# Kernel optimization log

Measured on AMD Instinct MI355X. Metric: run time of the kernel, lower is better.

The kernel has to match this reference:

```python
import jax, jax.numpy as jnp
import numpy as np
import math

B, LQ, LK, D, H = 4, 1024, 1024, 1024, 16
DK = D // H
SCALE = 1.0 / math.sqrt(DK)
NEG_INF = -1.0e9


def setup_inputs() -> dict:
    key = jax.random.key(0)
    ks = jax.random.split(key, 18)
    w = lambda k: (jax.random.normal(k, (D, D), dtype=jnp.float32) * 0.02)
    b = lambda k: (jax.random.normal(k, (D,), dtype=jnp.float32) * 0.02)
    mask = jax.random.randint(ks[4], (B, 1, LK), 0, 2).astype(jnp.int32)
    mask = mask.at[..., 0].set(1)  # ensure at least one valid key per row
    return {
        "query": jax.random.normal(ks[0], (B, LQ, D), dtype=jnp.float32),
        "key": jax.random.normal(ks[1], (B, LK, D), dtype=jnp.float32),
        "value": jax.random.normal(ks[2], (B, LK, D), dtype=jnp.float32),
        "weak_rela": jax.random.normal(ks[3], (B, LK, D), dtype=jnp.float32),
        "mask": mask,
        "Wq": w(ks[5]), "bq": b(ks[6]),
        "Wk": w(ks[7]), "bk": b(ks[8]),
        "Wv": w(ks[9]), "bv": b(ks[10]),
        "Wrk": w(ks[11]), "brk": b(ks[12]),
        "Wrv": w(ks[13]), "brv": b(ks[14]),
        "Wo": w(ks[15]), "bo": b(ks[16]),
    }


def _proj(x, W, bias):
    # x: [B, L, D] -> [B, H, L, DK]; torch Linear: y = x @ W.T + b
    y = x @ W.T + bias
    Bn, L, _ = y.shape
    return y.reshape(Bn, L, H, DK).transpose(0, 2, 1, 3)


def reference(query, key, value, weak_rela, mask,
              Wq, bq, Wk, bk, Wv, bv, Wrk, brk, Wrv, brv, Wo, bo):
    q = _proj(query, Wq, bq)        # [B,H,LQ,DK]
    k = _proj(key, Wk, bk)          # [B,H,LK,DK]
    v = _proj(value, Wv, bv)        # [B,H,LK,DK]
    rk = _proj(weak_rela, Wrk, brk) # [B,H,LK,DK]
    rv = _proj(weak_rela, Wrv, brv) # [B,H,LK,DK]

    qk = jnp.einsum('bhqd,bhkd->bhqk', q, k) * SCALE
    qr = jnp.einsum('bhqd,bhkd->bhqk', q, rk) * SCALE

    m = (mask[:, None, :, :] == 0)  # [B,1,1,LK] broadcast over heads/queries
    qk = jnp.where(m, NEG_INF, qk)
    qr = jnp.where(m, NEG_INF, qr)

    p_vis = jax.nn.softmax(qk, axis=-1)
    p_rel = jax.nn.softmax(qr, axis=-1)

    x = (jnp.einsum('bhqk,bhkd->bhqd', p_vis, v)
         + jnp.einsum('bhqk,bhkd->bhqd', p_rel, rv))  # [B,H,LQ,DK]
    x = x.transpose(0, 2, 1, 3).reshape(query.shape[0], -1, H * DK)
    return x @ Wo.T + bo
```

## Files before the change

### kernel.cpp

```cpp
#include <hip/hip_runtime.h>
#include <stdint.h>

#define NB 4
#define NH 16
#define DKH 64
#define DMODEL 1024
#define SEQ 1024
#define SCALE 0.125f
#define NEG_INF -1.0e9f
#define K2E 0.18033688011112042f

typedef __bf16 bf16_t;
typedef __bf16 bf16x8 __attribute__((ext_vector_type(8)));
typedef __bf16 bf16x4v __attribute__((ext_vector_type(4)));
typedef float f32x4 __attribute__((ext_vector_type(4)));
typedef uint32_t u32x4 __attribute__((ext_vector_type(4)));

typedef const uint32_t __attribute__((address_space(1)))* gas_ptr;
typedef uint32_t __attribute__((address_space(3)))* las_ptr;

__device__ __forceinline__ void gload_lds16(const void* g, void* l) {
  __builtin_amdgcn_global_load_lds((gas_ptr)g, (las_ptr)l, 16, 0, 0);
}


#define NXE ((size_t)NB * SEQ * DMODEL)
#define NWE ((size_t)DMODEL * DMODEL)

__global__ void cvt_all(const float* __restrict__ x0, const float* __restrict__ x1,
                        const float* __restrict__ x2, const float* __restrict__ x3,
                        const float* __restrict__ w0, const float* __restrict__ w1,
                        const float* __restrict__ w2, const float* __restrict__ w3,
                        const float* __restrict__ w4, const float* __restrict__ w5,
                        bf16_t* __restrict__ Xbase, bf16_t* __restrict__ Wbase) {
  const int y = blockIdx.y;
  const float* in;
  bf16_t* out;
  int n;
  if (y < 4) {
    in = (y == 0) ? x0 : (y == 1) ? x1 : (y == 2) ? x2 : x3;
    out = Xbase + (size_t)y * NXE;
    n = (int)NXE;
  } else {
    const int j = y - 4;
    in = (j == 0) ? w0 : (j == 1) ? w1 : (j == 2) ? w2 : (j == 3) ? w3 : (j == 4) ? w4 : w5;
    out = Wbase + (size_t)j * NWE;
    n = (int)NWE;
  }
  const int idx = (blockIdx.x * 256 + threadIdx.x) * 4;
  if (idx >= n) return;
  const float4 v = *(const float4*)(in + idx);
  bf16x4v p;
  p[0] = (bf16_t)v.x; p[1] = (bf16_t)v.y; p[2] = (bf16_t)v.z; p[3] = (bf16_t)v.w;
  *(bf16x4v*)(out + idx) = p;
}

template<int MODE>
__device__ __forceinline__ void gemm128_body(
    const bf16_t* __restrict__ A, const bf16_t* __restrict__ W,
    const float* __restrict__ bias, void* __restrict__ outp,
    int m0, int n0, bf16_t* As, bf16_t* Bs) {
  const int tid = threadIdx.x;
  const int lane = tid & 63;
  const int w = tid >> 6;
  const int wm = w >> 1, wn = w & 1;
  const int g = lane >> 4, c = lane & 15;
  const int lrow = lane >> 3;
  const int lcol = ((lane & 7) * 8) ^ ((lane >> 3) << 3);
  const int sc = (c & 7) << 3;

  f32x4 acc[4][4] = {};

  for (int kt = 0; kt < DMODEL; kt += 64) {
#pragma unroll
    for (int p = 0; p < 4; ++p) {
      const int row = w * 32 + p * 8;
      gload_lds16(A + (size_t)(m0 + row + lrow) * DMODEL + kt + lcol, &As[row * 64]);
      gload_lds16(W + (size_t)(n0 + row + lrow) * DMODEL + kt + lcol, &Bs[row * 64]);
    }
    __syncthreads();
    bf16x8 af[4][2], bfr[4][2];
#pragma unroll
    for (int i = 0; i < 4; ++i)
#pragma unroll
      for (int kk = 0; kk < 2; ++kk) {
        af[i][kk]  = *(const bf16x8*)&As[(wm * 64 + i * 16 + c) * 64 + ((kk * 32 + g * 8) ^ sc)];
        bfr[i][kk] = *(const bf16x8*)&Bs[(wn * 64 + i * 16 + c) * 64 + ((kk * 32 + g * 8) ^ sc)];
      }
#pragma unroll
    for (int i = 0; i < 4; ++i)
#pragma unroll
      for (int j = 0; j < 4; ++j) {
        acc[i][j] = __builtin_amdgcn_mfma_f32_16x16x32_bf16(af[i][0], bfr[j][0], acc[i][j], 0, 0, 0);
        acc[i][j] = __builtin_amdgcn_mfma_f32_16x16x32_bf16(af[i][1], bfr[j][1], acc[i][j], 0, 0, 0);
      }
    __syncthreads();
  }

  float bv4[4];
#pragma unroll
  for (int j = 0; j < 4; ++j) bv4[j] = bias[n0 + wn * 64 + j * 16 + c];

#pragma unroll
  for (int i = 0; i < 4; ++i) {
    const int mrow = m0 + wm * 64 + i * 16 + g * 4;
    const int b_ = mrow >> 10, l_ = mrow & 1023;
#pragma unroll
    for (int j = 0; j < 4; ++j) {
      const int n = n0 + wn * 64 + j * 16 + c;
      if (MODE == 0) {
        bf16_t* o = (bf16_t*)outp;
        const int h_ = n >> 6, dk_ = n & 63;
#pragma unroll
        for (int r = 0; r < 4; ++r)
          o[((size_t)(b_ * NH + h_) * SEQ + l_ + r) * DKH + dk_] =
              (bf16_t)(acc[i][j][r] + bv4[j]);
      } else {
        bf16_t* o = (bf16_t*)outp;
        const int h_ = n >> 6, dk_ = n & 63;
        bf16x4v pk;
#pragma unroll
        for (int r = 0; r < 4; ++r) pk[r] = (bf16_t)(acc[i][j][r] + bv4[j]);
        *(bf16x4v*)&o[((size_t)(b_ * NH + h_) * DKH + dk_) * SEQ + l_] = pk;
      }
    }
  }
}

__global__ void __launch_bounds__(256, 2)
proj_gemm(const bf16_t* __restrict__ Xbase, const bf16_t* __restrict__ Wbase,
          bf16_t* __restrict__ Obase,
          const float* __restrict__ b0, const float* __restrict__ b1,
          const float* __restrict__ b2, const float* __restrict__ b3,
          const float* __restrict__ b4) {
  __shared__ bf16_t As[128 * 64];
  __shared__ bf16_t Bs[128 * 64];
  const int bid = blockIdx.x;
  const int lid = (bid & 7) * 160 + (bid >> 3);
  const int seg = lid >> 8;
  const int rr = lid & 255;
  const int m0 = (rr >> 3) * 128, n0 = (rr & 7) * 128;

  const bf16_t* A = Xbase + (size_t)((seg < 3) ? seg : 3) * NXE;
  const bf16_t* W = Wbase + (size_t)seg * NWE;
  const int ooff = (seg == 0) ? 0 : (seg == 1) ? 1 : (seg == 2) ? 3 : (seg == 3) ? 2 : 4;
  bf16_t* out = Obase + (size_t)ooff * NXE;
  const float* bias = (seg == 0) ? b0 : (seg == 1) ? b1 : (seg == 2) ? b2 : (seg == 3) ? b3 : b4;

  if (seg == 2 || seg == 4) gemm128_body<1>(A, W, bias, out, m0, n0, As, Bs);
  else                      gemm128_body<0>(A, W, bias, out, m0, n0, As, Bs);
}

__global__ void __launch_bounds__(256, 2)
out_gemm(const bf16_t* __restrict__ A, const bf16_t* __restrict__ W,
         const float* __restrict__ bias, float* __restrict__ out) {
  __shared__ bf16_t As[128 * 64];
  __shared__ bf16_t Bs[64 * 64];
  const int tid = threadIdx.x;
  const int lane = tid & 63;
  const int w = tid >> 6;
  const int wm = w >> 1, wn = w & 1;
  const int g = lane >> 4, c = lane & 15;
  const int bid = blockIdx.x;
  const int lid = (bid & 7) * 64 + (bid >> 3);
  const int bm = lid >> 4, bn = lid & 15;
  const int m0 = bm * 128, n0 = bn * 64;
  const int lrow = lane >> 3;
  const int lcol = ((lane & 7) * 8) ^ ((lane >> 3) << 3);
  const int sc = (c & 7) << 3;

  f32x4 acc[4][2] = {};

  for (int kt = 0; kt < DMODEL; kt += 64) {
#pragma unroll
    for (int p = 0; p < 4; ++p) {
      const int row = w * 32 + p * 8;
      gload_lds16(A + (size_t)(m0 + row + lrow) * DMODEL + kt + lcol, &As[row * 64]);
    }
#pragma unroll
    for (int p = 0; p < 2; ++p) {
      const int row = w * 16 + p * 8;
      gload_lds16(W + (size_t)(n0 + row + lrow) * DMODEL + kt + lcol, &Bs[row * 64]);
    }
    __syncthreads();
    bf16x8 af[4][2], bfr[2][2];
#pragma unroll
    for (int i = 0; i < 4; ++i)
#pragma unroll
      for (int kk = 0; kk < 2; ++kk)
        af[i][kk] = *(const bf16x8*)&As[(wm * 64 + i * 16 + c) * 64 + ((kk * 32 + g * 8) ^ sc)];
#pragma unroll
    for (int j = 0; j < 2; ++j)
#pragma unroll
      for (int kk = 0; kk < 2; ++kk)
        bfr[j][kk] = *(const bf16x8*)&Bs[(wn * 32 + j * 16 + c) * 64 + ((kk * 32 + g * 8) ^ sc)];
#pragma unroll
    for (int i = 0; i < 4; ++i)
#pragma unroll
      for (int j = 0; j < 2; ++j) {
        acc[i][j] = __builtin_amdgcn_mfma_f32_16x16x32_bf16(af[i][0], bfr[j][0], acc[i][j], 0, 0, 0);
        acc[i][j] = __builtin_amdgcn_mfma_f32_16x16x32_bf16(af[i][1], bfr[j][1], acc[i][j], 0, 0, 0);
      }
    __syncthreads();
  }

  float bv2[2];
#pragma unroll
  for (int j = 0; j < 2; ++j) bv2[j] = bias[n0 + wn * 32 + j * 16 + c];
#pragma unroll
  for (int i = 0; i < 4; ++i) {
    const int mrow = m0 + wm * 64 + i * 16 + g * 4;
#pragma unroll
    for (int j = 0; j < 2; ++j) {
      const int n = n0 + wn * 32 + j * 16 + c;
#pragma unroll
      for (int r = 0; r < 4; ++r)
        out[(size_t)(mrow + r) * DMODEL + n] = acc[i][j][r] + bv2[j];
    }
  }
}

__global__ void __launch_bounds__(256, 2)
attn_kernel(const bf16_t* __restrict__ q, const bf16_t* __restrict__ k,
            const bf16_t* __restrict__ rk, const bf16_t* __restrict__ vT,
            const bf16_t* __restrict__ rvT, const int* __restrict__ mask,
            bf16_t* __restrict__ x) {
  extern __shared__ __align__(256) bf16_t smem[];
  bf16_t* Ks  = smem;
  bf16_t* RKs = Ks  + 64 * 64;
  bf16_t* Vs  = RKs + 64 * 64;
  bf16_t* RVs = Vs  + 64 * 64;
  bf16_t* Pbase = RVs + 64 * 64;
  float* Mb = (float*)(Pbase + 8 * 2048);

  const int tid = threadIdx.x;
  const int lane = tid & 63;
  const int w = tid >> 6;
  const int g = lane >> 4, c = lane & 15;
  const int sc = (c & 7) << 3;
  const int bid = blockIdx.x;
  const int lid = (bid & 7) * 64 + (bid >> 3);
  const int qt = lid & 7;
  const int bh = lid >> 3;
  const int b = bh >> 4, h = bh & 15;
  const int q0 = qt * 128;

  const bf16_t* qp = q + (size_t)bh * SEQ * DKH;
  const bf16_t* kp = k + (size_t)bh * SEQ * DKH;
  const bf16_t* rkp = rk + (size_t)bh * SEQ * DKH;
  const bf16_t* vp = vT + (size_t)bh * DKH * SEQ;
  const bf16_t* rvp = rvT + (size_t)bh * DKH * SEQ;
  const int* mp = mask + b * SEQ;

  const int lrow = lane >> 3;
  const int lcolL = (lane & 7) * 8;
  const int wcol = lcolL ^ (((w * 16 + lrow) & 7) << 3);

  bf16_t* Pwv = Pbase + w * 2048;
  bf16_t* Pwr = Pbase + (4 + w) * 2048;

#pragma unroll
  for (int i = 0; i < 4; ++i) {
    const int idx = i * 256 + tid;
    Mb[idx] = (mp[idx] == 0) ? NEG_INF : 0.0f;
  }

  bf16x8 qf[2][2];
#pragma unroll
  for (int i = 0; i < 2; ++i)
#pragma unroll
    for (int kk = 0; kk < 2; ++kk)
      qf[i][kk] = *(const bf16x8*)(qp + (size_t)(q0 + w * 32 + i * 16 + c) * DKH + kk * 32 + g * 8);

  f32x4 ov[2][4] = {}, orl[2][4] = {};
  float mv[2] = {NEG_INF, NEG_INF}, mr[2] = {NEG_INF, NEG_INF};
  float lv[2] = {0.f, 0.f}, lr[2] = {0.f, 0.f};

  u32x4 st[4][2];

  auto ldreg = [&](int kv0) {
#pragma unroll
    for (int p = 0; p < 2; ++p) {
      const int row = w * 16 + p * 8 + lrow;
      st[0][p] = *(const u32x4*)(kp  + (size_t)(kv0 + row) * DKH + lcolL);
      st[1][p] = *(const u32x4*)(rkp + (size_t)(kv0 + row) * DKH + lcolL);
      st[2][p] = *(const u32x4*)(vp  + (size_t)row * SEQ + kv0 + lcolL);
      st[3][p] = *(const u32x4*)(rvp + (size_t)row * SEQ + kv0 + lcolL);
    }
  };
  auto wrlds = [&]() {
#pragma unroll
    for (int p = 0; p < 2; ++p) {
      const int row = w * 16 + p * 8 + lrow;
      *(u32x4*)&Ks [row * 64 + wcol] = st[0][p];
      *(u32x4*)&RKs[row * 64 + wcol] = st[1][p];
      *(u32x4*)&Vs [row * 64 + wcol] = st[2][p];
      *(u32x4*)&RVs[row * 64 + wcol] = st[3][p];
    }
  };

  auto qk_sm = [&](const bf16_t* Kt, bf16_t* Pb, const f32x4 (&mb)[4],
                   float (&m_s)[2], float (&l_s)[2], f32x4 (&o_s)[2][4]) {
    f32x4 s[2][4];
    {
      bf16x8 kfr[4][2];
#pragma unroll
      for (int f = 0; f < 4; ++f) {
        kfr[f][0] = *(const bf16x8*)&Kt[(f * 16 + c) * 64 + ((g * 8) ^ sc)];
        kfr[f][1] = *(const bf16x8*)&Kt[(f * 16 + c) * 64 + ((32 + g * 8) ^ sc)];
      }
      __builtin_amdgcn_s_setprio(1);
#pragma unroll
      for (int i = 0; i < 2; ++i)
#pragma unroll
        for (int f = 0; f < 4; ++f) {
          f32x4 a = {0.f, 0.f, 0.f, 0.f};
          a = __builtin_amdgcn_mfma_f32_16x16x32_bf16(kfr[f][0], qf[i][0], a, 0, 0, 0);
          a = __builtin_amdgcn_mfma_f32_16x16x32_bf16(kfr[f][1], qf[i][1], a, 0, 0, 0);
          s[i][f] = a;
        }
      __builtin_amdgcn_s_setprio(0);
    }

#pragma unroll
    for (int i = 0; i < 2; ++i)
#pragma unroll
      for (int f = 0; f < 4; ++f)
#pragma unroll
        for (int r = 0; r < 4; ++r)
          s[i][f][r] = s[i][f][r] * K2E + mb[f][r];

#pragma unroll
    for (int i = 0; i < 2; ++i) {
      float tm = fmaxf(fmaxf(s[i][0][0], s[i][0][1]), fmaxf(s[i][0][2], s[i][0][3]));
#pragma unroll
      for (int f = 1; f < 4; ++f)
        tm = fmaxf(tm, fmaxf(fmaxf(s[i][f][0], s[i][f][1]), fmaxf(s[i][f][2], s[i][f][3])));
      tm = fmaxf(tm, __shfl_xor(tm, 16));
      tm = fmaxf(tm, __shfl_xor(tm, 32));
      if (!__all(tm <= m_s[i] + 8.0f)) {
        const float mnew = fmaxf(m_s[i], tm);
        const float sf = __builtin_amdgcn_exp2f(m_s[i] - mnew);
        m_s[i] = mnew;
        l_s[i] *= sf;
#pragma unroll
        for (int jd = 0; jd < 4; ++jd)
#pragma unroll
          for (int r = 0; r < 4; ++r) o_s[i][jd][r] *= sf;
      }
      float pf = 0.f;
#pragma unroll
      for (int f = 0; f < 4; ++f) {
        bf16x4v pk;
#pragma unroll
        for (int r = 0; r < 4; ++r) {
          const float p = __builtin_amdgcn_exp2f(s[i][f][r] - m_s[i]);
          pf += p;
          pk[r] = (bf16_t)p;
        }
        *(bf16x4v*)&Pb[i * 1024 + c * 64 + ((f * 16 + g * 4) ^ sc)] = pk;
      }
      l_s[i] += pf;
    }
  };

  auto pv = [&](const bf16_t* Vt, const bf16_t* Pb, f32x4 (&o_s)[2][4]) {
    bf16x8 pa[2][2];
#pragma unroll
    for (int i = 0; i < 2; ++i) {
      pa[i][0] = *(const bf16x8*)&Pb[i * 1024 + c * 64 + ((g * 8) ^ sc)];
      pa[i][1] = *(const bf16x8*)&Pb[i * 1024 + c * 64 + ((32 + g * 8) ^ sc)];
    }
#pragma unroll
    for (int jd = 0; jd < 4; ++jd) {
      const bf16x8 v0 = *(const bf16x8*)&Vt[(jd * 16 + c) * 64 + ((g * 8) ^ sc)];
      const bf16x8 v1 = *(const bf16x8*)&Vt[(jd * 16 + c) * 64 + ((32 + g * 8) ^ sc)];
#pragma unroll
      for (int i = 0; i < 2; ++i) {
        o_s[i][jd] = __builtin_amdgcn_mfma_f32_16x16x32_bf16(v0, pa[i][0], o_s[i][jd], 0, 0, 0);
        o_s[i][jd] = __builtin_amdgcn_mfma_f32_16x16x32_bf16(v1, pa[i][1], o_s[i][jd], 0, 0, 0);
      }
    }
  };

  ldreg(0);
  wrlds();
  __syncthreads();

  for (int t = 0; t < 16; ++t) {
    const int kv0 = t * 64;

    if (t < 15) ldreg(kv0 + 64);

    f32x4 mb[4];
#pragma unroll
    for (int f = 0; f < 4; ++f)
      mb[f] = *(const f32x4*)&Mb[kv0 + f * 16 + g * 4];

    qk_sm(Ks,  Pwv, mb, mv, lv, ov);
    qk_sm(RKs, Pwr, mb, mr, lr, orl);
    __builtin_amdgcn_s_setprio(1);
    pv(Vs,  Pwv, ov);
    pv(RVs, Pwr, orl);
    __builtin_amdgcn_s_setprio(0);

    if (t < 15) {
      __syncthreads();
      wrlds();
      __syncthreads();
    }
  }

#pragma unroll
  for (int i = 0; i < 2; ++i) {
    lv[i] += __shfl_xor(lv[i], 16); lv[i] += __shfl_xor(lv[i], 32);
    lr[i] += __shfl_xor(lr[i], 16); lr[i] += __shfl_xor(lr[i], 32);
  }

  bf16_t* xb = x + (size_t)b * SEQ * DMODEL + (size_t)h * DKH;
#pragma unroll
  for (int i = 0; i < 2; ++i) {
    const float rlv = 1.0f / lv[i], rlr = 1.0f / lr[i];
    const int qrow = q0 + w * 32 + i * 16 + c;
#pragma unroll
    for (int jd = 0; jd < 4; ++jd) {
      bf16x4v pk;
#pragma unroll
      for (int r = 0; r < 4; ++r)
        pk[r] = (bf16_t)(ov[i][jd][r] * rlv + orl[i][jd][r] * rlr);
      *(bf16x4v*)&xb[(size_t)qrow * DMODEL + jd * 16 + g * 4] = pk;
    }
  }
}

extern "C" void kernel_launch(void* const* d_in, const int* in_sizes, int n_in,
                              void* d_out, int out_size, void* d_ws, size_t ws_size,
                              hipStream_t stream) {
  (void)in_sizes; (void)n_in; (void)out_size; (void)ws_size;
  const float* query = (const float*)d_in[0];
  const float* key_  = (const float*)d_in[1];
  const float* value = (const float*)d_in[2];
  const float* weak  = (const float*)d_in[3];
  const int*   mask  = (const int*)d_in[4];
  const float* Wq  = (const float*)d_in[5];  const float* bq  = (const float*)d_in[6];
  const float* Wk  = (const float*)d_in[7];  const float* bk  = (const float*)d_in[8];
  const float* Wv  = (const float*)d_in[9];  const float* bv  = (const float*)d_in[10];
  const float* Wrk = (const float*)d_in[11]; const float* brk = (const float*)d_in[12];
  const float* Wrv = (const float*)d_in[13]; const float* brv = (const float*)d_in[14];
  const float* Wo  = (const float*)d_in[15]; const float* bo  = (const float*)d_in[16];

  char* ws = (char*)d_ws;
  size_t off = 0;
  auto alloc = [&](size_t bytes) {
    void* p = ws + off;
    off += (bytes + 255) & ~(size_t)255;
    return p;
  };
  const size_t SZ_X = NXE * sizeof(bf16_t);
  const size_t SZ_W = NWE * sizeof(bf16_t);

  bf16_t* Xq = (bf16_t*)alloc(SZ_X);
  bf16_t* Xk = (bf16_t*)alloc(SZ_X);
  bf16_t* Xv = (bf16_t*)alloc(SZ_X);
  bf16_t* Xr = (bf16_t*)alloc(SZ_X);
  bf16_t* Wqb  = (bf16_t*)alloc(SZ_W);
  bf16_t* Wkb  = (bf16_t*)alloc(SZ_W);
  bf16_t* Wvb  = (bf16_t*)alloc(SZ_W);
  bf16_t* Wrkb = (bf16_t*)alloc(SZ_W);
  bf16_t* Wrvb = (bf16_t*)alloc(SZ_W);
  bf16_t* Wob  = (bf16_t*)alloc(SZ_W);
  bf16_t* qh   = (bf16_t*)alloc(SZ_X);
  bf16_t* kh   = (bf16_t*)alloc(SZ_X);
  bf16_t* rkh  = (bf16_t*)alloc(SZ_X);
  bf16_t* vTh  = (bf16_t*)alloc(SZ_X);
  bf16_t* rvTh = (bf16_t*)alloc(SZ_X);
  bf16_t* xh   = (bf16_t*)alloc(SZ_X);
  (void)Xk; (void)Xv; (void)Xr; (void)Wkb; (void)Wvb; (void)Wrkb; (void)Wrvb;
  (void)kh; (void)rkh; (void)vTh; (void)rvTh;

  cvt_all<<<dim3(4096, 10), 256, 0, stream>>>(query, key_, value, weak,
                                              Wq, Wk, Wv, Wrk, Wrv, Wo,
                                              Xq, Wqb);

  proj_gemm<<<dim3(1280), 256, 0, stream>>>(Xq, Wqb, qh, bq, bk, bv, brk, brv);

  attn_kernel<<<dim3(512), 256, 69632, stream>>>(qh, kh, rkh, vTh, rvTh, mask, xh);

  out_gemm<<<dim3(512), 256, 0, stream>>>(xh, Wob, bo, (float*)d_out);
}
```

Baseline: 161.7 us.

## Double-buffer K/V tiles in LDS with two-deep register prefetch

The attention loop now ping-pongs between two LDS buffers holding K, RK, V and RV. It prefetches global tiles two steps ahead into registers, which cuts the two barriers per iteration down to one. The mask is read from global into registers and turned into bias values each step, replacing the LDS mask table. The visible and relation branches now run qk then pv in sequence and share one per-wave P buffer. LDS use rises to 80 KB per block, which leaves only just enough room for two blocks per CU, and register pressure goes up from the extra prefetch state.

```diff
diff --git a/kernel.cpp b/kernel.cpp
--- a/kernel.cpp
+++ b/kernel.cpp
@@ -226,12 +226,7 @@
             const bf16_t* __restrict__ rvT, const int* __restrict__ mask,
             bf16_t* __restrict__ x) {
   extern __shared__ __align__(256) bf16_t smem[];
-  bf16_t* Ks  = smem;
-  bf16_t* RKs = Ks  + 64 * 64;
-  bf16_t* Vs  = RKs + 64 * 64;
-  bf16_t* RVs = Vs  + 64 * 64;
-  bf16_t* Pbase = RVs + 64 * 64;
-  float* Mb = (float*)(Pbase + 8 * 2048);
+  bf16_t* Pbase = smem + 2 * 16384;
 
   const int tid = threadIdx.x;
   const int lane = tid & 63;
@@ -256,14 +251,7 @@
   const int lcolL = (lane & 7) * 8;
   const int wcol = lcolL ^ (((w * 16 + lrow) & 7) << 3);
 
-  bf16_t* Pwv = Pbase + w * 2048;
-  bf16_t* Pwr = Pbase + (4 + w) * 2048;
-
-#pragma unroll
-  for (int i = 0; i < 4; ++i) {
-    const int idx = i * 256 + tid;
-    Mb[idx] = (mp[idx] == 0) ? NEG_INF : 0.0f;
-  }
+  bf16_t* Pw = Pbase + w * 2048;
 
   bf16x8 qf[2][2];
 #pragma unroll
@@ -277,6 +265,8 @@
   float lv[2] = {0.f, 0.f}, lr[2] = {0.f, 0.f};
 
   u32x4 st[4][2];
+  int4 st_m[4];
+  int4 mk[4];
 
   auto ldreg = [&](int kv0) {
 #pragma unroll
@@ -287,19 +277,22 @@
       st[2][p] = *(const u32x4*)(vp  + (size_t)row * SEQ + kv0 + lcolL);
       st[3][p] = *(const u32x4*)(rvp + (size_t)row * SEQ + kv0 + lcolL);
     }
-  };
-  auto wrlds = [&]() {
+#pragma unroll
+    for (int f = 0; f < 4; ++f)
+      st_m[f] = *(const int4*)&mp[kv0 + f * 16 + g * 4];
+  };
+  auto wrlds = [&](bf16_t* buf) {
 #pragma unroll
     for (int p = 0; p < 2; ++p) {
       const int row = w * 16 + p * 8 + lrow;
-      *(u32x4*)&Ks [row * 64 + wcol] = st[0][p];
-      *(u32x4*)&RKs[row * 64 + wcol] = st[1][p];
-      *(u32x4*)&Vs [row * 64 + wcol] = st[2][p];
-      *(u32x4*)&RVs[row * 64 + wcol] = st[3][p];
-    }
-  };
-
-  auto qk_sm = [&](const bf16_t* Kt, bf16_t* Pb, const f32x4 (&mb)[4],
+      *(u32x4*)&buf[0 * 4096 + row * 64 + wcol] = st[0][p];
+      *(u32x4*)&buf[1 * 4096 + row * 64 + wcol] = st[1][p];
+      *(u32x4*)&buf[2 * 4096 + row * 64 + wcol] = st[2][p];
+      *(u32x4*)&buf[3 * 4096 + row * 64 + wcol] = st[3][p];
+    }
+  };
+
+  auto qk_sm = [&](const bf16_t* Kt, const f32x4 (&mb)[4],
                    float (&m_s)[2], float (&l_s)[2], f32x4 (&o_s)[2][4]) {
     f32x4 s[2][4];
     {
@@ -309,7 +302,6 @@
         kfr[f][0] = *(const bf16x8*)&Kt[(f * 16 + c) * 64 + ((g * 8) ^ sc)];
         kfr[f][1] = *(const bf16x8*)&Kt[(f * 16 + c) * 64 + ((32 + g * 8) ^ sc)];
       }
-      __builtin_amdgcn_s_setprio(1);
 #pragma unroll
       for (int i = 0; i < 2; ++i)
 #pragma unroll
@@ -319,7 +311,6 @@
           a = __builtin_amdgcn_mfma_f32_16x16x32_bf16(kfr[f][1], qf[i][1], a, 0, 0, 0);
           s[i][f] = a;
         }
-      __builtin_amdgcn_s_setprio(0);
     }
 
 #pragma unroll
@@ -358,18 +349,18 @@
           pf += p;
           pk[r] = (bf16_t)p;
         }
-        *(bf16x4v*)&Pb[i * 1024 + c * 64 + ((f * 16 + g * 4) ^ sc)] = pk;
+        *(bf16x4v*)&Pw[i * 1024 + c * 64 + ((f * 16 + g * 4) ^ sc)] = pk;
       }
       l_s[i] += pf;
     }
   };
 
-  auto pv = [&](const bf16_t* Vt, const bf16_t* Pb, f32x4 (&o_s)[2][4]) {
+  auto pv = [&](const bf16_t* Vt, f32x4 (&o_s)[2][4]) {
     bf16x8 pa[2][2];
 #pragma unroll
     for (int i = 0; i < 2; ++i) {
-      pa[i][0] = *(const bf16x8*)&Pb[i * 1024 + c * 64 + ((g * 8) ^ sc)];
-      pa[i][1] = *(const bf16x8*)&Pb[i * 1024 + c * 64 + ((32 + g * 8) ^ sc)];
+      pa[i][0] = *(const bf16x8*)&Pw[i * 1024 + c * 64 + ((g * 8) ^ sc)];
+      pa[i][1] = *(const bf16x8*)&Pw[i * 1024 + c * 64 + ((32 + g * 8) ^ sc)];
     }
 #pragma unroll
     for (int jd = 0; jd < 4; ++jd) {
@@ -383,32 +374,48 @@
     }
   };
 
+  auto step = [&](int t, const bf16_t* CUR, bf16_t* OTH) {
+    if (t < 15) wrlds(OTH);
+
+    f32x4 mb[4];
+#pragma unroll
+    for (int f = 0; f < 4; ++f) {
+      mb[f][0] = mk[f].x ? 0.f : NEG_INF;
+      mb[f][1] = mk[f].y ? 0.f : NEG_INF;
+      mb[f][2] = mk[f].z ? 0.f : NEG_INF;
+      mb[f][3] = mk[f].w ? 0.f : NEG_INF;
+    }
+    if (t < 15) {
+#pragma unroll
+      for (int f = 0; f < 4; ++f) mk[f] = st_m[f];
+    }
+    if (t < 14) ldreg((t + 2) * 64);
+
+    qk_sm(CUR, mb, mv, lv, ov);
+    __builtin_amdgcn_s_setprio(1);
+    pv(CUR + 2 * 4096, ov);
+    __builtin_amdgcn_s_setprio(0);
+    qk_sm(CUR + 1 * 4096, mb, mr, lr, orl);
+    __builtin_amdgcn_s_setprio(1);
+    pv(CUR + 3 * 4096, orl);
+    __builtin_amdgcn_s_setprio(0);
+
+    __syncthreads();
+  };
+
+  bf16_t* bufA = smem;
+  bf16_t* bufB = smem + 16384;
+
   ldreg(0);
-  wrlds();
+  wrlds(bufA);
+#pragma unroll
+  for (int f = 0; f < 4; ++f) mk[f] = st_m[f];
+  ldreg(64);
   __syncthreads();
 
-  for (int t = 0; t < 16; ++t) {
-    const int kv0 = t * 64;
-
-    if (t < 15) ldreg(kv0 + 64);
-
-    f32x4 mb[4];
-#pragma unroll
-    for (int f = 0; f < 4; ++f)
-      mb[f] = *(const f32x4*)&Mb[kv0 + f * 16 + g * 4];
-
-    qk_sm(Ks,  Pwv, mb, mv, lv, ov);
-    qk_sm(RKs, Pwr, mb, mr, lr, orl);
-    __builtin_amdgcn_s_setprio(1);
-    pv(Vs,  Pwv, ov);
-    pv(RVs, Pwr, orl);
-    __builtin_amdgcn_s_setprio(0);
-
-    if (t < 15) {
-      __syncthreads();
-      wrlds();
-      __syncthreads();
-    }
+  for (int tt = 0; tt < 8; ++tt) {
+    step(tt * 2,     bufA, bufB);
+    step(tt * 2 + 1, bufB, bufA);
   }
 
 #pragma unroll
@@ -484,7 +491,7 @@
 
   proj_gemm<<<dim3(1280), 256, 0, stream>>>(Xq, Wqb, qh, bq, bk, bv, brk, brv);
 
-  attn_kernel<<<dim3(512), 256, 69632, stream>>>(qh, kh, rkh, vTh, rvTh, mask, xh);
+  attn_kernel<<<dim3(512), 256, 81920, stream>>>(qh, kh, rkh, vTh, rvTh, mask, xh);
 
   out_gemm<<<dim3(512), 256, 0, stream>>>(xh, Wob, bo, (float*)d_out);
 }
```

Measured after the change: 245.7 us. 1.52x slower.
